# Kernel tuning notes

Measured on AMD Instinct MI355X. Metric: run time of the kernel, lower is better.

## Reference

```python
import jax, jax.numpy as jnp
import numpy as np

L, H, E, CUTOFF = 3, 128, 20, 5.0
N_NODES, N_EDGES = 10000, 160000
NUM_EMBED = 119


def _linear(key, fin, fout):
    kw, kb = jax.random.split(key)
    s = 1.0 / np.sqrt(fin)
    W = jax.random.uniform(kw, (fin, fout), minval=-s, maxval=s, dtype=jnp.float32)
    b = jax.random.uniform(kb, (fout,), minval=-s, maxval=s, dtype=jnp.float32)
    return W, b


def _stack(key, fin, fout):
    Ws, bs = zip(*[_linear(k, fin, fout) for k in jax.random.split(key, L)])
    return jnp.stack(Ws), jnp.stack(bs)


def setup_inputs() -> dict:
    key = jax.random.key(0)
    ks = jax.random.split(key, 14)
    z = jax.random.randint(ks[0], (N_NODES,), 0, NUM_EMBED)
    edge = jax.random.randint(ks[1], (N_EDGES, 2), 0, N_NODES)
    edge_diff = jax.random.normal(ks[2], (N_EDGES, 3), dtype=jnp.float32) * 1.5
    edge_dist = jnp.linalg.norm(edge_diff, axis=-1) + 1e-2  # consistent unit vectors, strictly > 0
    embed = jax.random.normal(ks[3], (NUM_EMBED, H), dtype=jnp.float32)
    msg_filter_w, msg_filter_b = _stack(ks[4], E, 3 * H)
    msg_w1, msg_b1 = _stack(ks[5], H, H)
    msg_w2, msg_b2 = _stack(ks[6], H, 3 * H)
    upd_U_w, upd_U_b = _stack(ks[7], H, H)
    upd_V_w, upd_V_b = _stack(ks[8], H, H)
    upd_w1, upd_b1 = _stack(ks[9], 2 * H, H)
    upd_w2, upd_b2 = _stack(ks[10], H, 3 * H)
    ro_w1, ro_b1 = _linear(ks[11], H, H)
    ro_w2, ro_b2 = _linear(ks[12], H, H)
    return dict(z=z, edge=edge, edge_diff=edge_diff, edge_dist=edge_dist, embed=embed,
                msg_filter_w=msg_filter_w, msg_filter_b=msg_filter_b,
                msg_w1=msg_w1, msg_b1=msg_b1, msg_w2=msg_w2, msg_b2=msg_b2,
                upd_U_w=upd_U_w, upd_U_b=upd_U_b, upd_V_w=upd_V_w, upd_V_b=upd_V_b,
                upd_w1=upd_w1, upd_b1=upd_b1, upd_w2=upd_w2, upd_b2=upd_b2,
                ro_w1=ro_w1, ro_b1=ro_b1, ro_w2=ro_w2, ro_b2=ro_b2)


def _silu(x):
    return x * jax.nn.sigmoid(x)


def reference(z, edge, edge_diff, edge_dist, embed,
              msg_filter_w, msg_filter_b, msg_w1, msg_b1, msg_w2, msg_b2,
              upd_U_w, upd_U_b, upd_V_w, upd_V_b, upd_w1, upd_b1, upd_w2, upd_b2,
              ro_w1, ro_b1, ro_w2, ro_b2):
    N = z.shape[0]
    pi = jnp.asarray(np.pi, dtype=edge_dist.dtype)
    # sinc radial basis: sin(n*pi*d/cutoff)/d, n=1..E  -> [E_edges, E]
    n = jnp.arange(1, E + 1, dtype=edge_dist.dtype)
    rbf = jnp.sin(edge_dist[:, None] * n * pi / CUTOFF) / edge_dist[:, None]
    # cosine cutoff [E_edges]
    fcut = jnp.where(edge_dist < CUTOFF, 0.5 * (jnp.cos(pi * edge_dist / CUTOFF) + 1.0), 0.0)
    unit = edge_diff / edge_dist[:, None]  # [E_edges, 3]
    src = edge[:, 1]
    dst = edge[:, 0]

    node_scalar = embed[z]                                       # [N, H]
    node_vector = jnp.zeros((N, 3, H), dtype=edge_diff.dtype)    # [N, 3, H]

    for l in range(L):
        # --- message ---
        filter_w = (rbf @ msg_filter_w[l] + msg_filter_b[l]) * fcut[:, None]   # [E_edges, 3H]
        scalar_out = _silu(node_scalar @ msg_w1[l] + msg_b1[l]) @ msg_w2[l] + msg_b2[l]  # [N, 3H]
        filter_out = filter_w * scalar_out[src]                                 # gather + mul
        gate_sv, gate_ev, msg_s = jnp.split(filter_out, 3, axis=1)
        msg_v = node_vector[src] * gate_sv[:, None, :] + gate_ev[:, None, :] * unit[:, :, None]
        node_scalar = node_scalar + jax.ops.segment_sum(msg_s, dst, num_segments=N)
        node_vector = node_vector + jax.ops.segment_sum(msg_v, dst, num_segments=N)
        # --- update ---
        Uv = node_vector @ upd_U_w[l] + upd_U_b[l]   # [N, 3, H]
        Vv = node_vector @ upd_V_w[l] + upd_V_b[l]
        Vv_norm = jnp.linalg.norm(Vv, axis=1)        # [N, H]
        mlp_in = jnp.concatenate((Vv_norm, node_scalar), axis=1)
        mlp_out = _silu(mlp_in @ upd_w1[l] + upd_b1[l]) @ upd_w2[l] + upd_b2[l]
        a_vv, a_sv, a_ss = jnp.split(mlp_out, 3, axis=1)
        node_vector = node_vector + a_vv[:, None, :] * Uv
        node_scalar = node_scalar + a_sv * jnp.sum(Uv * Vv, axis=1) + a_ss

    # readout MLP
    return _silu(node_scalar @ ro_w1 + ro_b1) @ ro_w2 + ro_b2
```

## Files before the change

kernel.cpp:

```cpp
#include <hip/hip_runtime.h>
#include <hip/hip_bf16.h>

typedef __hip_bfloat16 bf16;
typedef __attribute__((ext_vector_type(8))) short bf16x8;
typedef __attribute__((ext_vector_type(4))) float f32x4;

#define H 128
#define F3H 384
#define E_RBF 20
#define NLAYER 3

__device__ __forceinline__ float silu_f(float x) { return x / (1.0f + __expf(-x)); }
__device__ __forceinline__ float b2f(bf16 x) { return __bfloat162float(x); }

constexpr float PI_F = 3.14159265358979323846f;
constexpr float CUT = 5.0f;

__global__ __launch_bounds__(256) void csr_hist(
    const int* __restrict__ edge, int* __restrict__ cnt, int nE) {
  int e = blockIdx.x * blockDim.x + threadIdx.x;
  if (e < nE) atomicAdd(&cnt[edge[2 * e]], 1);
}

__global__ __launch_bounds__(1024) void csr_scan(
    const int* __restrict__ cnt, int* __restrict__ rowstart, int* __restrict__ cur, int N) {
  __shared__ int part[1024];
  int t = threadIdx.x;
  int chunk = (N + 1023) / 1024;
  int lo = t * chunk; if (lo > N) lo = N;
  int hi = lo + chunk; if (hi > N) hi = N;
  int s = 0;
  for (int i = lo; i < hi; i++) s += cnt[i];
  part[t] = s;
  __syncthreads();
  for (int off = 1; off < 1024; off <<= 1) {
    int v = (t >= off) ? part[t - off] : 0;
    __syncthreads();
    part[t] += v;
    __syncthreads();
  }
  int r = (t == 0) ? 0 : part[t - 1];
  for (int i = lo; i < hi; i++) { rowstart[i] = r; cur[i] = r; r += cnt[i]; }
}

__global__ __launch_bounds__(256) void csr_fill_pack(
    const int* __restrict__ edge, int* __restrict__ cur,
    const float* __restrict__ edist, const float* __restrict__ ediff,
    int* __restrict__ srcs, float* __restrict__ geo, int nE) {
  int e = blockIdx.x * blockDim.x + threadIdx.x;
  if (e >= nE) return;
  int d = edge[2 * e];
  int p = atomicAdd(&cur[d], 1);
  srcs[p] = edge[2 * e + 1];
  float dd = edist[e];
  float inv = 1.0f / dd;
  float th = dd * (PI_F / CUT);
  float s1 = sinf(th), c1 = cosf(th);
  float fc = (dd < CUT) ? 0.5f * (c1 + 1.0f) : 0.0f;
  float* g = geo + (size_t)p * 24;
  float twoc = 2.0f * c1;
  float skp = 0.0f, sk = s1;
  #pragma unroll
  for (int k = 0; k < E_RBF; k++) {
    g[k] = sk * inv * fc;
    float nx = twoc * sk - skp;
    skp = sk; sk = nx;
  }
  g[20] = ediff[3 * (size_t)e] * inv;
  g[21] = ediff[3 * (size_t)e + 1] * inv;
  g[22] = ediff[3 * (size_t)e + 2] * inv;
  g[23] = fc;
}

__device__ __forceinline__ void pack_w_item(
    const float* __restrict__ Wu, const float* __restrict__ Wv,
    bf16* __restrict__ wp, int t) {
  int lane = t & 63;
  int c    = (t >> 6) & 7;
  int kb   = (t >> 9) & 3;
  int mat  = (t >> 11) & 1;
  int l    = t >> 12;
  const float* src = (mat ? Wv : Wu) + (size_t)l * H * H;
  bf16* dst = wp + ((size_t)(l * 2 + mat) * 16384) + (((kb * 8 + c) * 64 + lane) * 8);
  int quad = lane >> 4;
  int n = c * 16 + (lane & 15);
  #pragma unroll
  for (int j = 0; j < 8; j++) {
    int k = kb * 32 + quad * 8 + j;
    dst[j] = __float2bfloat16(src[(size_t)k * H + n]);
  }
}

__device__ __forceinline__ void pack_b_item(
    const float* __restrict__ src, bf16* __restrict__ dst,
    int K, int ncols, int t) {
  int kblocks = K >> 5, ncols16 = ncols >> 4;
  int lane = t & 63;
  int idx = t >> 6;
  int c = idx % ncols16; idx /= ncols16;
  int kb = idx % kblocks; idx /= kblocks;
  int l = idx;
  const float* s = src + (size_t)l * K * ncols;
  bf16* d = dst + (size_t)l * K * ncols + (((kb * ncols16 + c) * 64 + lane) * 8);
  int quad = lane >> 4;
  int n = c * 16 + (lane & 15);
  #pragma unroll
  for (int j = 0; j < 8; j++) {
    int k = kb * 32 + quad * 8 + j;
    d[j] = __float2bfloat16(s[(size_t)k * ncols + n]);
  }
}

__global__ __launch_bounds__(256) void pack_all(
    const float* __restrict__ Wu, const float* __restrict__ Wv, bf16* __restrict__ wpack,
    const float* __restrict__ uw1, bf16* __restrict__ wp_m1,
    const float* __restrict__ uw2, bf16* __restrict__ wp_m2,
    const float* __restrict__ mw1, bf16* __restrict__ wp_sm1,
    const float* __restrict__ mw2, bf16* __restrict__ wp_sm2,
    const float* __restrict__ rw1, bf16* __restrict__ wp_ro1,
    const float* __restrict__ rw2, bf16* __restrict__ wp_ro2,
    const int* __restrict__ z, const float* __restrict__ embed,
    float* __restrict__ ns, bf16* __restrict__ ns16,
    int* __restrict__ cnt, int N) {
  const int T0 = 12288;
  const int T1 = T0 + 12288;
  const int T2 = T1 + 18432;
  const int T3 = T2 + 6144;
  const int T4 = T3 + 18432;
  const int T5 = T4 + 2048;
  const int T6 = T5 + 2048;
  const int TN = T6 + N * H;
  const int TT = TN + N;
  for (int t = blockIdx.x * blockDim.x + threadIdx.x; t < TT; t += gridDim.x * blockDim.x) {
    if (t < T0)      pack_w_item(Wu, Wv, wpack, t);
    else if (t < T1) pack_b_item(uw1, wp_m1, 256, 128, t - T0);
    else if (t < T2) pack_b_item(uw2, wp_m2, 128, 384, t - T1);
    else if (t < T3) pack_b_item(mw1, wp_sm1, 128, 128, t - T2);
    else if (t < T4) pack_b_item(mw2, wp_sm2, 128, 384, t - T3);
    else if (t < T5) pack_b_item(rw1, wp_ro1, 128, 128, t - T4);
    else if (t < T6) pack_b_item(rw2, wp_ro2, 128, 128, t - T5);
    else if (t < TN) {
      int u = t - T6;
      int i = u >> 7, h = u & 127;
      float v = embed[(size_t)z[i] * H + h];
      ns[(size_t)i * H + h] = v;
      ns16[(size_t)i * H + h] = __float2bfloat16(v);
    } else {
      cnt[t - TN] = 0;
    }
  }
}

__global__ __launch_bounds__(256) void mlp_msg(
    const bf16* __restrict__ A, const bf16* __restrict__ Wp1,
    const float* __restrict__ b1, const bf16* __restrict__ Wp2,
    const float* __restrict__ b2, bf16* __restrict__ so, int M) {
  __shared__ bf16 m1l[32][136];
  int wave = threadIdx.x >> 6, lane = threadIdx.x & 63;
  int rowg = wave >> 1, ch = wave & 1;
  int r0 = blockIdx.x * 32 + rowg * 16;
  int quad = lane >> 4, nn = lane & 15;
  int arow = r0 + nn; if (arow >= M) arow = M - 1;
  f32x4 acc[4] = {};
  for (int kb = 0; kb < 4; kb++) {
    bf16x8 af = *(const bf16x8*)&A[(size_t)arow * H + kb * 32 + quad * 8];
    #pragma unroll
    for (int c = 0; c < 4; c++) {
      int cg = ch * 4 + c;
      bf16x8 bw = *(const bf16x8*)&Wp1[(((kb * 8 + cg) * 64) + lane) * 8];
      acc[c] = __builtin_amdgcn_mfma_f32_16x16x32_bf16(af, bw, acc[c], 0, 0, 0);
    }
  }
  #pragma unroll
  for (int c = 0; c < 4; c++) {
    int n = (ch * 4 + c) * 16 + nn;
    float bb = b1[n];
    #pragma unroll
    for (int r = 0; r < 4; r++) {
      int lr = rowg * 16 + quad * 4 + r;
      m1l[lr][n] = __float2bfloat16(silu_f(acc[c][r] + bb));
    }
  }
  __syncthreads();
  f32x4 a0[4] = {}, a1[4] = {}, a2[4] = {};
  for (int kb = 0; kb < 4; kb++) {
    bf16x8 af = *(const bf16x8*)&m1l[rowg * 16 + nn][kb * 32 + quad * 8];
    #pragma unroll
    for (int c = 0; c < 4; c++) {
      int cg = ch * 4 + c;
      bf16x8 b0 = *(const bf16x8*)&Wp2[(((kb * 24 + cg) * 64) + lane) * 8];
      bf16x8 b1v = *(const bf16x8*)&Wp2[(((kb * 24 + cg + 8) * 64) + lane) * 8];
      bf16x8 b2v = *(const bf16x8*)&Wp2[(((kb * 24 + cg + 16) * 64) + lane) * 8];
      a0[c] = __builtin_amdgcn_mfma_f32_16x16x32_bf16(af, b0, a0[c], 0, 0, 0);
      a1[c] = __builtin_amdgcn_mfma_f32_16x16x32_bf16(af, b1v, a1[c], 0, 0, 0);
      a2[c] = __builtin_amdgcn_mfma_f32_16x16x32_bf16(af, b2v, a2[c], 0, 0, 0);
    }
  }
  #pragma unroll
  for (int c = 0; c < 4; c++) {
    int n = (ch * 4 + c) * 16 + nn;
    float bb0 = b2[n], bb1 = b2[H + n], bb2 = b2[2 * H + n];
    #pragma unroll
    for (int r = 0; r < 4; r++) {
      int row = r0 + quad * 4 + r;
      if (row < M) {
        so[(size_t)row * F3H + n]           = __float2bfloat16(a0[c][r] + bb0);
        so[(size_t)row * F3H + H + n]       = __float2bfloat16(a1[c][r] + bb1);
        so[(size_t)row * F3H + 2 * H + n]   = __float2bfloat16(a2[c][r] + bb2);
      }
    }
  }
}

__global__ __launch_bounds__(384) void uv_upd(
    const bf16* __restrict__ A, const bf16* __restrict__ Wpuv,
    const float* __restrict__ bu, const float* __restrict__ bv,
    const bf16* __restrict__ nsmsg,
    const bf16* __restrict__ Wp1, const float* __restrict__ b1,
    const bf16* __restrict__ Wp2, const float* __restrict__ b2,
    float* __restrict__ ns, bf16* __restrict__ ns16,
    float* __restrict__ nv, bf16* __restrict__ nvb16, int N) {
  __shared__ float Uv_l[96][132];
  __shared__ float Vv_l[96][132];
  __shared__ bf16 vn_l[32][136];
  __shared__ bf16 m1l[32][136];
  int wave = threadIdx.x >> 6;
  int lane = threadIdx.x & 63;
  int quad = lane >> 4, nn = lane & 15;
  int M3 = 3 * N;

  {
    int r0 = blockIdx.x * 96 + wave * 16;
    int arow = r0 + nn; if (arow >= M3) arow = M3 - 1;
    f32x4 accu[8] = {};
    f32x4 accv[8] = {};
    for (int kb = 0; kb < 4; kb++) {
      bf16x8 af = *(const bf16x8*)&A[(size_t)arow * H + kb * 32 + quad * 8];
      #pragma unroll
      for (int c = 0; c < 8; c++) {
        bf16x8 bfu = *(const bf16x8*)&Wpuv[(((kb * 8 + c) * 64) + lane) * 8];
        bf16x8 bfv = *(const bf16x8*)&Wpuv[16384 + (((kb * 8 + c) * 64) + lane) * 8];
        accu[c] = __builtin_amdgcn_mfma_f32_16x16x32_bf16(af, bfu, accu[c], 0, 0, 0);
        accv[c] = __builtin_amdgcn_mfma_f32_16x16x32_bf16(af, bfv, accv[c], 0, 0, 0);
      }
    }
    #pragma unroll
    for (int c = 0; c < 8; c++) {
      int n = c * 16 + nn;
      float bub = bu[n], bvb = bv[n];
      #pragma unroll
      for (int r = 0; r < 4; r++) {
        int lr = wave * 16 + quad * 4 + r;
        Uv_l[lr][n] = accu[c][r] + bub;
        Vv_l[lr][n] = accv[c][r] + bvb;
      }
    }
  }
  __syncthreads();

  for (int t = threadIdx.x; t < 32 * H; t += 384) {
    int node = t >> 7, hh = t & 127;
    float v0 = Vv_l[node * 3][hh];
    float v1 = Vv_l[node * 3 + 1][hh];
    float v2 = Vv_l[node * 3 + 2][hh];
    vn_l[node][hh] = __float2bfloat16(sqrtf(v0 * v0 + v1 * v1 + v2 * v2));
  }
  __syncthreads();

  int rowg = wave >> 1, ch = wave & 1;
  int r0n = blockIdx.x * 32 + rowg * 16;
  int arown = r0n + nn; if (arown >= N) arown = N - 1;
  if (wave < 4) {
    f32x4 acc[4] = {};
    for (int kb = 0; kb < 8; kb++) {
      bf16x8 af;
      if (kb < 4) af = *(const bf16x8*)&vn_l[rowg * 16 + nn][kb * 32 + quad * 8];
      else        af = *(const bf16x8*)&nsmsg[(size_t)arown * H + (kb - 4) * 32 + quad * 8];
      #pragma unroll
      for (int c = 0; c < 4; c++) {
        int cg = ch * 4 + c;
        bf16x8 bw = *(const bf16x8*)&Wp1[(((kb * 8 + cg) * 64) + lane) * 8];
        acc[c] = __builtin_amdgcn_mfma_f32_16x16x32_bf16(af, bw, acc[c], 0, 0, 0);
      }
    }
    #pragma unroll
    for (int c = 0; c < 4; c++) {
      int n = (ch * 4 + c) * 16 + nn;
      float bb = b1[n];
      #pragma unroll
      for (int r = 0; r < 4; r++) {
        int lr = rowg * 16 + quad * 4 + r;
        m1l[lr][n] = __float2bfloat16(silu_f(acc[c][r] + bb));
      }
    }
  }
  __syncthreads();

  if (wave < 4) {
    f32x4 aav[4] = {}, aas[4] = {}, asz[4] = {};
    for (int kb = 0; kb < 4; kb++) {
      bf16x8 af = *(const bf16x8*)&m1l[rowg * 16 + nn][kb * 32 + quad * 8];
      #pragma unroll
      for (int c = 0; c < 4; c++) {
        int cg = ch * 4 + c;
        bf16x8 b0 = *(const bf16x8*)&Wp2[(((kb * 24 + cg) * 64) + lane) * 8];
        bf16x8 b1v = *(const bf16x8*)&Wp2[(((kb * 24 + cg + 8) * 64) + lane) * 8];
        bf16x8 b2v = *(const bf16x8*)&Wp2[(((kb * 24 + cg + 16) * 64) + lane) * 8];
        aav[c] = __builtin_amdgcn_mfma_f32_16x16x32_bf16(af, b0, aav[c], 0, 0, 0);
        aas[c] = __builtin_amdgcn_mfma_f32_16x16x32_bf16(af, b1v, aas[c], 0, 0, 0);
        asz[c] = __builtin_amdgcn_mfma_f32_16x16x32_bf16(af, b2v, asz[c], 0, 0, 0);
      }
    }
    #pragma unroll
    for (int c = 0; c < 4; c++) {
      int n = (ch * 4 + c) * 16 + nn;
      float bav = b2[n], bas = b2[H + n], bss = b2[2 * H + n];
      #pragma unroll
      for (int r = 0; r < 4; r++) {
        int row = r0n + quad * 4 + r;
        if (row < N) {
          int lrn = rowg * 16 + quad * 4 + r;
          float avv = aav[c][r] + bav;
          float asv = aas[c][r] + bas;
          float ass = asz[c][r] + bss;
          float u0 = Uv_l[lrn * 3 + 0][n];
          float u1 = Uv_l[lrn * 3 + 1][n];
          float u2 = Uv_l[lrn * 3 + 2][n];
          float v0 = Vv_l[lrn * 3 + 0][n];
          float v1 = Vv_l[lrn * 3 + 1][n];
          float v2 = Vv_l[lrn * 3 + 2][n];
          float dot = u0 * v0 + u1 * v1 + u2 * v2;
          float ns_new = ns[(size_t)row * H + n] + asv * dot + ass;
          ns[(size_t)row * H + n] = ns_new;
          ns16[(size_t)row * H + n] = __float2bfloat16(ns_new);
          float n0 = nv[(size_t)(3 * row + 0) * H + n] + avv * u0;
          float n1 = nv[(size_t)(3 * row + 1) * H + n] + avv * u1;
          float n2 = nv[(size_t)(3 * row + 2) * H + n] + avv * u2;
          nv[(size_t)(3 * row + 0) * H + n] = n0;
          nv[(size_t)(3 * row + 1) * H + n] = n1;
          nv[(size_t)(3 * row + 2) * H + n] = n2;
          nvb16[(size_t)(3 * row + 0) * H + n] = __float2bfloat16(n0);
          nvb16[(size_t)(3 * row + 1) * H + n] = __float2bfloat16(n1);
          nvb16[(size_t)(3 * row + 2) * H + n] = __float2bfloat16(n2);
        }
      }
    }
  }
}

__global__ __launch_bounds__(256) void mlp_ro(
    const bf16* __restrict__ A, const bf16* __restrict__ Wp1,
    const float* __restrict__ b1, const bf16* __restrict__ Wp2,
    const float* __restrict__ b2, float* __restrict__ out, int M) {
  __shared__ bf16 m1l[32][136];
  int wave = threadIdx.x >> 6, lane = threadIdx.x & 63;
  int rowg = wave >> 1, ch = wave & 1;
  int r0 = blockIdx.x * 32 + rowg * 16;
  int quad = lane >> 4, nn = lane & 15;
  int arow = r0 + nn; if (arow >= M) arow = M - 1;
  f32x4 acc[4] = {};
  for (int kb = 0; kb < 4; kb++) {
    bf16x8 af = *(const bf16x8*)&A[(size_t)arow * H + kb * 32 + quad * 8];
    #pragma unroll
    for (int c = 0; c < 4; c++) {
      int cg = ch * 4 + c;
      bf16x8 bw = *(const bf16x8*)&Wp1[(((kb * 8 + cg) * 64) + lane) * 8];
      acc[c] = __builtin_amdgcn_mfma_f32_16x16x32_bf16(af, bw, acc[c], 0, 0, 0);
    }
  }
  #pragma unroll
  for (int c = 0; c < 4; c++) {
    int n = (ch * 4 + c) * 16 + nn;
    float bb = b1[n];
    #pragma unroll
    for (int r = 0; r < 4; r++) {
      int lr = rowg * 16 + quad * 4 + r;
      m1l[lr][n] = __float2bfloat16(silu_f(acc[c][r] + bb));
    }
  }
  __syncthreads();
  f32x4 a2[4] = {};
  for (int kb = 0; kb < 4; kb++) {
    bf16x8 af = *(const bf16x8*)&m1l[rowg * 16 + nn][kb * 32 + quad * 8];
    #pragma unroll
    for (int c = 0; c < 4; c++) {
      int cg = ch * 4 + c;
      bf16x8 bw = *(const bf16x8*)&Wp2[(((kb * 8 + cg) * 64) + lane) * 8];
      a2[c] = __builtin_amdgcn_mfma_f32_16x16x32_bf16(af, bw, a2[c], 0, 0, 0);
    }
  }
  #pragma unroll
  for (int c = 0; c < 4; c++) {
    int n = (ch * 4 + c) * 16 + nn;
    float bb = b2[n];
    #pragma unroll
    for (int r = 0; r < 4; r++) {
      int row = r0 + quad * 4 + r;
      if (row < M) out[(size_t)row * H + n] = a2[c][r] + bb;
    }
  }
}

template<bool HASNV>
__global__ __launch_bounds__(128, 4) void message3(
    const int* __restrict__ srcs, const int* __restrict__ rowstart,
    const int* __restrict__ cnt, const float* __restrict__ geo,
    const float* __restrict__ Wf, const float* __restrict__ bfb,
    const bf16* __restrict__ so, const bf16* __restrict__ nvb16,
    const float* __restrict__ nvA,
    float* __restrict__ ns, float* __restrict__ nvB,
    bf16* __restrict__ nvmsg16, bf16* __restrict__ nsmsg, int N) {
  int i = blockIdx.x;
  int h = threadIdx.x;

  float wf0[E_RBF], wf1[E_RBF], wf2[E_RBF];
  #pragma unroll
  for (int k = 0; k < E_RBF; k++) {
    wf0[k] = Wf[k * F3H + h];
    wf1[k] = Wf[k * F3H + H + h];
    wf2[k] = Wf[k * F3H + 2 * H + h];
  }
  float bb0 = bfb[h], bb1 = bfb[H + h], bb2 = bfb[2 * H + h];

  float accs = 0.0f, a0 = 0.0f, a1 = 0.0f, a2 = 0.0f;
  int jlo = rowstart[i], jhi = jlo + cnt[i];
  int j = jlo;
  for (; j + 1 < jhi; j += 2) {
    int s0 = srcs[j];
    int s1 = srcs[j + 1];
    const bf16* sop0 = so + (size_t)s0 * F3H;
    const bf16* sop1 = so + (size_t)s1 * F3H;
    float sA0 = b2f(sop0[h]), sB0 = b2f(sop0[H + h]), sC0 = b2f(sop0[2 * H + h]);
    float sA1 = b2f(sop1[h]), sB1 = b2f(sop1[H + h]), sC1 = b2f(sop1[2 * H + h]);
    float nA0, nB0, nC0, nA1, nB1, nC1;
    if (HASNV) {
      const bf16* nvp0 = nvb16 + (size_t)s0 * F3H;
      const bf16* nvp1 = nvb16 + (size_t)s1 * F3H;
      nA0 = b2f(nvp0[h]); nB0 = b2f(nvp0[H + h]); nC0 = b2f(nvp0[2 * H + h]);
      nA1 = b2f(nvp1[h]); nB1 = b2f(nvp1[H + h]); nC1 = b2f(nvp1[2 * H + h]);
    }

    {
      const float* g = geo + (size_t)j * 24;
      float gg[24];
      #pragma unroll
      for (int q = 0; q < 6; q++) *(float4*)&gg[4 * q] = *(const float4*)&g[4 * q];
      float fc = gg[23];
      float f0 = bb0 * fc, f1 = bb1 * fc, f2 = bb2 * fc;
      #pragma unroll
      for (int k = 0; k < E_RBF; k++) {
        float rk = gg[k];
        f0 += rk * wf0[k];
        f1 += rk * wf1[k];
        f2 += rk * wf2[k];
      }
      float u0 = gg[20], u1 = gg[21], u2 = gg[22];
      float gsv = f0 * sA0;
      float gev = f1 * sB0;
      accs += f2 * sC0;
      if (HASNV) {
        a0 += nA0 * gsv + gev * u0;
        a1 += nB0 * gsv + gev * u1;
        a2 += nC0 * gsv + gev * u2;
      } else {
        a0 += gev * u0;
        a1 += gev * u1;
        a2 += gev * u2;
      }
    }
    {
      const float* g = geo + (size_t)(j + 1) * 24;
      float gg[24];
      #pragma unroll
      for (int q = 0; q < 6; q++) *(float4*)&gg[4 * q] = *(const float4*)&g[4 * q];
      float fc = gg[23];
      float f0 = bb0 * fc, f1 = bb1 * fc, f2 = bb2 * fc;
      #pragma unroll
      for (int k = 0; k < E_RBF; k++) {
        float rk = gg[k];
        f0 += rk * wf0[k];
        f1 += rk * wf1[k];
        f2 += rk * wf2[k];
      }
      float u0 = gg[20], u1 = gg[21], u2 = gg[22];
      float gsv = f0 * sA1;
      float gev = f1 * sB1;
      accs += f2 * sC1;
      if (HASNV) {
        a0 += nA1 * gsv + gev * u0;
        a1 += nB1 * gsv + gev * u1;
        a2 += nC1 * gsv + gev * u2;
      } else {
        a0 += gev * u0;
        a1 += gev * u1;
        a2 += gev * u2;
      }
    }
  }
  if (j < jhi) {
    int src = srcs[j];
    const float* g = geo + (size_t)j * 24;
    float gg[24];
    #pragma unroll
    for (int q = 0; q < 6; q++) *(float4*)&gg[4 * q] = *(const float4*)&g[4 * q];
    float fc = gg[23];
    float f0 = bb0 * fc, f1 = bb1 * fc, f2 = bb2 * fc;
    #pragma unroll
    for (int k = 0; k < E_RBF; k++) {
      float rk = gg[k];
      f0 += rk * wf0[k];
      f1 += rk * wf1[k];
      f2 += rk * wf2[k];
    }
    float u0 = gg[20], u1 = gg[21], u2 = gg[22];
    const bf16* sop = so + (size_t)src * F3H;
    float gsv = f0 * b2f(sop[h]);
    float gev = f1 * b2f(sop[H + h]);
    accs += f2 * b2f(sop[2 * H + h]);
    if (HASNV) {
      const bf16* nvp = nvb16 + (size_t)src * F3H;
      a0 += b2f(nvp[h])         * gsv + gev * u0;
      a1 += b2f(nvp[H + h])     * gsv + gev * u1;
      a2 += b2f(nvp[2 * H + h]) * gsv + gev * u2;
    } else {
      a0 += gev * u0;
      a1 += gev * u1;
      a2 += gev * u2;
    }
  }

  float ns_new = ns[(size_t)i * H + h] + accs;
  ns[(size_t)i * H + h] = ns_new;
  nsmsg[(size_t)i * H + h] = __float2bfloat16(ns_new);
  float o0, o1, o2;
  if (HASNV) {
    const float* nvi = nvA + (size_t)i * F3H;
    o0 = nvi[h] + a0;
    o1 = nvi[H + h] + a1;
    o2 = nvi[2 * H + h] + a2;
  } else {
    o0 = a0; o1 = a1; o2 = a2;
  }
  nvB[(size_t)i * F3H + h]         = o0;
  nvB[(size_t)i * F3H + H + h]     = o1;
  nvB[(size_t)i * F3H + 2 * H + h] = o2;
  nvmsg16[(size_t)i * F3H + h]         = __float2bfloat16(o0);
  nvmsg16[(size_t)i * F3H + H + h]     = __float2bfloat16(o1);
  nvmsg16[(size_t)i * F3H + 2 * H + h] = __float2bfloat16(o2);
}

extern "C" void kernel_launch(void* const* d_in, const int* in_sizes, int n_in,
                              void* d_out, int out_size, void* d_ws, size_t ws_size,
                              hipStream_t stream) {
  const int*   z     = (const int*)d_in[0];
  const int*   edge  = (const int*)d_in[1];
  const float* ediff = (const float*)d_in[2];
  const float* edist = (const float*)d_in[3];
  const float* embed = (const float*)d_in[4];
  const float* mfw   = (const float*)d_in[5];
  const float* mfb   = (const float*)d_in[6];
  const float* mw1   = (const float*)d_in[7];
  const float* mb1   = (const float*)d_in[8];
  const float* mw2   = (const float*)d_in[9];
  const float* mb2   = (const float*)d_in[10];
  const float* uUw   = (const float*)d_in[11];
  const float* uUb   = (const float*)d_in[12];
  const float* uVw   = (const float*)d_in[13];
  const float* uVb   = (const float*)d_in[14];
  const float* uw1   = (const float*)d_in[15];
  const float* ub1   = (const float*)d_in[16];
  const float* uw2   = (const float*)d_in[17];
  const float* ub2   = (const float*)d_in[18];
  const float* rw1   = (const float*)d_in[19];
  const float* rb1   = (const float*)d_in[20];
  const float* rw2   = (const float*)d_in[21];
  const float* rb2   = (const float*)d_in[22];

  const int N  = in_sizes[0];
  const int nE = in_sizes[3];

  float* ws = (float*)d_ws;
  size_t off = 0;
  float* ns      = ws + off; off += (size_t)N * H;
  float* nvA     = ws + off; off += (size_t)N * F3H;
  float* nvB     = ws + off; off += (size_t)N * F3H;
  float* geo     = ws + off; off += (size_t)nE * 24;
  bf16* so       = (bf16*)(ws + off); off += (size_t)N * F3H / 2;
  bf16* nvb16    = (bf16*)(ws + off); off += (size_t)N * F3H / 2;
  bf16* nvmsg16  = (bf16*)(ws + off); off += (size_t)N * F3H / 2;
  bf16* nsmsg    = (bf16*)(ws + off); off += (size_t)N * 64;
  bf16* ns16     = (bf16*)(ws + off); off += (size_t)N * 64;
  bf16* wpack    = (bf16*)(ws + off); off += 3 * 2 * 16384 / 2;
  bf16* wp_m1    = (bf16*)(ws + off); off += 3 * 256 * 128 / 2;
  bf16* wp_m2    = (bf16*)(ws + off); off += 3 * 128 * 384 / 2;
  bf16* wp_sm1   = (bf16*)(ws + off); off += 3 * 128 * 128 / 2;
  bf16* wp_sm2   = (bf16*)(ws + off); off += 3 * 128 * 384 / 2;
  bf16* wp_ro1   = (bf16*)(ws + off); off += 128 * 128 / 2;
  bf16* wp_ro2   = (bf16*)(ws + off); off += 128 * 128 / 2;
  int* srcs     = (int*)(ws + off); off += nE;
  int* cnt      = (int*)(ws + off); off += N;
  int* rowstart = (int*)(ws + off); off += N;
  int* cur      = (int*)(ws + off); off += N;

  const int tilesN = (N + 31) / 32;

  pack_all<<<1024, 256, 0, stream>>>(
      uUw, uVw, wpack, uw1, wp_m1, uw2, wp_m2, mw1, wp_sm1, mw2, wp_sm2,
      rw1, wp_ro1, rw2, wp_ro2, z, embed, ns, ns16, cnt, N);
  csr_hist<<<(nE + 255) / 256, 256, 0, stream>>>(edge, cnt, nE);
  csr_scan<<<1, 1024, 0, stream>>>(cnt, rowstart, cur, N);
  csr_fill_pack<<<(nE + 255) / 256, 256, 0, stream>>>(edge, cur, edist, ediff, srcs, geo, nE);

  float* nv_cur = nvA;
  float* nv_nxt = nvB;
  for (int l = 0; l < NLAYER; l++) {
    mlp_msg<<<tilesN, 256, 0, stream>>>(
        ns16, wp_sm1 + (size_t)l * 128 * 128, mb1 + (size_t)l * H,
        wp_sm2 + (size_t)l * 128 * 384, mb2 + (size_t)l * F3H, so, N);

    if (l == 0)
      message3<false><<<N, H, 0, stream>>>(srcs, rowstart, cnt, geo,
                                           mfw + (size_t)l * E_RBF * F3H, mfb + (size_t)l * F3H,
                                           so, nvb16, nv_cur, ns, nv_nxt, nvmsg16, nsmsg, N);
    else
      message3<true><<<N, H, 0, stream>>>(srcs, rowstart, cnt, geo,
                                          mfw + (size_t)l * E_RBF * F3H, mfb + (size_t)l * F3H,
                                          so, nvb16, nv_cur, ns, nv_nxt, nvmsg16, nsmsg, N);

    uv_upd<<<tilesN, 384, 0, stream>>>(
        nvmsg16, wpack + (size_t)l * 2 * 16384,
        uUb + (size_t)l * H, uVb + (size_t)l * H,
        nsmsg,
        wp_m1 + (size_t)l * 256 * 128, ub1 + (size_t)l * H,
        wp_m2 + (size_t)l * 128 * 384, ub2 + (size_t)l * F3H,
        ns, ns16, nv_nxt, nvb16, N);

    float* t = nv_cur; nv_cur = nv_nxt; nv_nxt = t;
  }

  mlp_ro<<<tilesN, 256, 0, stream>>>(
      ns16, wp_ro1, rb1, wp_ro2, rb2, (float*)d_out, N);
}
```

Measured before the change: 483.2 us.

## Halve uv_upd tile to 16 nodes and split U/V GEMM across waves

The fused update kernel now handles 16 nodes per block instead of 32, doubling the grid and halving shared memory per block. The six waves are redistributed: three compute U and three compute V for the 48 vector rows, and all six waves share the eight column groups of the two MLP stages instead of only four waves working. Fewer accumulators per wave plus launch bounds of 3 blocks per CU aim to raise occupancy and parallelism. In exchange, each block reloads the weight fragments for half as many rows, and the MLP stages are unbalanced (two waves do two groups).

```diff
diff --git a/kernel.cpp b/kernel.cpp
--- a/kernel.cpp
+++ b/kernel.cpp
@@ -212,7 +212,7 @@
   }
 }
 
-__global__ __launch_bounds__(384) void uv_upd(
+__global__ __launch_bounds__(384, 3) void uv_upd(
     const bf16* __restrict__ A, const bf16* __restrict__ Wpuv,
     const float* __restrict__ bu, const float* __restrict__ bv,
     const bf16* __restrict__ nsmsg,
@@ -220,45 +220,46 @@
     const bf16* __restrict__ Wp2, const float* __restrict__ b2,
     float* __restrict__ ns, bf16* __restrict__ ns16,
     float* __restrict__ nv, bf16* __restrict__ nvb16, int N) {
-  __shared__ float Uv_l[96][132];
-  __shared__ float Vv_l[96][132];
-  __shared__ bf16 vn_l[32][136];
-  __shared__ bf16 m1l[32][136];
+  __shared__ float Uv_l[48][132];
+  __shared__ float Vv_l[48][132];
+  __shared__ bf16 vn_l[16][136];
+  __shared__ bf16 m1l[16][136];
   int wave = threadIdx.x >> 6;
   int lane = threadIdx.x & 63;
   int quad = lane >> 4, nn = lane & 15;
   int M3 = 3 * N;
 
   {
-    int r0 = blockIdx.x * 96 + wave * 16;
+    int wt = (wave >= 3) ? wave - 3 : wave;
+    bool isV = wave >= 3;
+    int r0 = blockIdx.x * 48 + wt * 16;
     int arow = r0 + nn; if (arow >= M3) arow = M3 - 1;
-    f32x4 accu[8] = {};
-    f32x4 accv[8] = {};
+    const bf16* Wb = Wpuv + (isV ? 16384 : 0);
+    f32x4 acc[8] = {};
     for (int kb = 0; kb < 4; kb++) {
       bf16x8 af = *(const bf16x8*)&A[(size_t)arow * H + kb * 32 + quad * 8];
       #pragma unroll
       for (int c = 0; c < 8; c++) {
-        bf16x8 bfu = *(const bf16x8*)&Wpuv[(((kb * 8 + c) * 64) + lane) * 8];
-        bf16x8 bfv = *(const bf16x8*)&Wpuv[16384 + (((kb * 8 + c) * 64) + lane) * 8];
-        accu[c] = __builtin_amdgcn_mfma_f32_16x16x32_bf16(af, bfu, accu[c], 0, 0, 0);
-        accv[c] = __builtin_amdgcn_mfma_f32_16x16x32_bf16(af, bfv, accv[c], 0, 0, 0);
-      }
-    }
+        bf16x8 bw = *(const bf16x8*)&Wb[(((kb * 8 + c) * 64) + lane) * 8];
+        acc[c] = __builtin_amdgcn_mfma_f32_16x16x32_bf16(af, bw, acc[c], 0, 0, 0);
+      }
+    }
+    const float* bias = isV ? bv : bu;
     #pragma unroll
     for (int c = 0; c < 8; c++) {
       int n = c * 16 + nn;
-      float bub = bu[n], bvb = bv[n];
+      float bb = bias[n];
       #pragma unroll
       for (int r = 0; r < 4; r++) {
-        int lr = wave * 16 + quad * 4 + r;
-        Uv_l[lr][n] = accu[c][r] + bub;
-        Vv_l[lr][n] = accv[c][r] + bvb;
+        int lr = wt * 16 + quad * 4 + r;
+        if (isV) Vv_l[lr][n] = acc[c][r] + bb;
+        else     Uv_l[lr][n] = acc[c][r] + bb;
       }
     }
   }
   __syncthreads();
 
-  for (int t = threadIdx.x; t < 32 * H; t += 384) {
+  for (int t = threadIdx.x; t < 16 * H; t += 384) {
     int node = t >> 7, hh = t & 127;
     float v0 = Vv_l[node * 3][hh];
     float v1 = Vv_l[node * 3 + 1][hh];
@@ -267,82 +268,66 @@
   }
   __syncthreads();
 
-  int rowg = wave >> 1, ch = wave & 1;
-  int r0n = blockIdx.x * 32 + rowg * 16;
+  int r0n = blockIdx.x * 16;
   int arown = r0n + nn; if (arown >= N) arown = N - 1;
-  if (wave < 4) {
-    f32x4 acc[4] = {};
+  for (int g = wave; g < 8; g += 6) {
+    f32x4 acc = {};
     for (int kb = 0; kb < 8; kb++) {
       bf16x8 af;
-      if (kb < 4) af = *(const bf16x8*)&vn_l[rowg * 16 + nn][kb * 32 + quad * 8];
+      if (kb < 4) af = *(const bf16x8*)&vn_l[nn][kb * 32 + quad * 8];
       else        af = *(const bf16x8*)&nsmsg[(size_t)arown * H + (kb - 4) * 32 + quad * 8];
-      #pragma unroll
-      for (int c = 0; c < 4; c++) {
-        int cg = ch * 4 + c;
-        bf16x8 bw = *(const bf16x8*)&Wp1[(((kb * 8 + cg) * 64) + lane) * 8];
-        acc[c] = __builtin_amdgcn_mfma_f32_16x16x32_bf16(af, bw, acc[c], 0, 0, 0);
-      }
-    }
-    #pragma unroll
-    for (int c = 0; c < 4; c++) {
-      int n = (ch * 4 + c) * 16 + nn;
-      float bb = b1[n];
-      #pragma unroll
-      for (int r = 0; r < 4; r++) {
-        int lr = rowg * 16 + quad * 4 + r;
-        m1l[lr][n] = __float2bfloat16(silu_f(acc[c][r] + bb));
-      }
+      bf16x8 bw = *(const bf16x8*)&Wp1[(((kb * 8 + g) * 64) + lane) * 8];
+      acc = __builtin_amdgcn_mfma_f32_16x16x32_bf16(af, bw, acc, 0, 0, 0);
+    }
+    int n = g * 16 + nn;
+    float bb = b1[n];
+    #pragma unroll
+    for (int r = 0; r < 4; r++) {
+      m1l[quad * 4 + r][n] = __float2bfloat16(silu_f(acc[r] + bb));
     }
   }
   __syncthreads();
 
-  if (wave < 4) {
-    f32x4 aav[4] = {}, aas[4] = {}, asz[4] = {};
+  for (int g = wave; g < 8; g += 6) {
+    f32x4 aav = {}, aas = {}, asz = {};
     for (int kb = 0; kb < 4; kb++) {
-      bf16x8 af = *(const bf16x8*)&m1l[rowg * 16 + nn][kb * 32 + quad * 8];
-      #pragma unroll
-      for (int c = 0; c < 4; c++) {
-        int cg = ch * 4 + c;
-        bf16x8 b0 = *(const bf16x8*)&Wp2[(((kb * 24 + cg) * 64) + lane) * 8];
-        bf16x8 b1v = *(const bf16x8*)&Wp2[(((kb * 24 + cg + 8) * 64) + lane) * 8];
-        bf16x8 b2v = *(const bf16x8*)&Wp2[(((kb * 24 + cg + 16) * 64) + lane) * 8];
-        aav[c] = __builtin_amdgcn_mfma_f32_16x16x32_bf16(af, b0, aav[c], 0, 0, 0);
-        aas[c] = __builtin_amdgcn_mfma_f32_16x16x32_bf16(af, b1v, aas[c], 0, 0, 0);
-        asz[c] = __builtin_amdgcn_mfma_f32_16x16x32_bf16(af, b2v, asz[c], 0, 0, 0);
-      }
-    }
-    #pragma unroll
-    for (int c = 0; c < 4; c++) {
-      int n = (ch * 4 + c) * 16 + nn;
-      float bav = b2[n], bas = b2[H + n], bss = b2[2 * H + n];
-      #pragma unroll
-      for (int r = 0; r < 4; r++) {
-        int row = r0n + quad * 4 + r;
-        if (row < N) {
-          int lrn = rowg * 16 + quad * 4 + r;
-          float avv = aav[c][r] + bav;
-          float asv = aas[c][r] + bas;
-          float ass = asz[c][r] + bss;
-          float u0 = Uv_l[lrn * 3 + 0][n];
-          float u1 = Uv_l[lrn * 3 + 1][n];
-          float u2 = Uv_l[lrn * 3 + 2][n];
-          float v0 = Vv_l[lrn * 3 + 0][n];
-          float v1 = Vv_l[lrn * 3 + 1][n];
-          float v2 = Vv_l[lrn * 3 + 2][n];
-          float dot = u0 * v0 + u1 * v1 + u2 * v2;
-          float ns_new = ns[(size_t)row * H + n] + asv * dot + ass;
-          ns[(size_t)row * H + n] = ns_new;
-          ns16[(size_t)row * H + n] = __float2bfloat16(ns_new);
-          float n0 = nv[(size_t)(3 * row + 0) * H + n] + avv * u0;
-          float n1 = nv[(size_t)(3 * row + 1) * H + n] + avv * u1;
-          float n2 = nv[(size_t)(3 * row + 2) * H + n] + avv * u2;
-          nv[(size_t)(3 * row + 0) * H + n] = n0;
-          nv[(size_t)(3 * row + 1) * H + n] = n1;
-          nv[(size_t)(3 * row + 2) * H + n] = n2;
-          nvb16[(size_t)(3 * row + 0) * H + n] = __float2bfloat16(n0);
-          nvb16[(size_t)(3 * row + 1) * H + n] = __float2bfloat16(n1);
-          nvb16[(size_t)(3 * row + 2) * H + n] = __float2bfloat16(n2);
-        }
+      bf16x8 af = *(const bf16x8*)&m1l[nn][kb * 32 + quad * 8];
+      bf16x8 b0 = *(const bf16x8*)&Wp2[(((kb * 24 + g) * 64) + lane) * 8];
+      bf16x8 b1v = *(const bf16x8*)&Wp2[(((kb * 24 + g + 8) * 64) + lane) * 8];
+      bf16x8 b2v = *(const bf16x8*)&Wp2[(((kb * 24 + g + 16) * 64) + lane) * 8];
+      aav = __builtin_amdgcn_mfma_f32_16x16x32_bf16(af, b0, aav, 0, 0, 0);
+      aas = __builtin_amdgcn_mfma_f32_16x16x32_bf16(af, b1v, aas, 0, 0, 0);
+      asz = __builtin_amdgcn_mfma_f32_16x16x32_bf16(af, b2v, asz, 0, 0, 0);
+    }
+    int n = g * 16 + nn;
+    float bav = b2[n], bas = b2[H + n], bss = b2[2 * H + n];
+    #pragma unroll
+    for (int r = 0; r < 4; r++) {
+      int row = r0n + quad * 4 + r;
+      if (row < N) {
+        int lrn = quad * 4 + r;
+        float avv = aav[r] + bav;
+        float asv = aas[r] + bas;
+        float ass = asz[r] + bss;
+        float u0 = Uv_l[lrn * 3 + 0][n];
+        float u1 = Uv_l[lrn * 3 + 1][n];
+        float u2 = Uv_l[lrn * 3 + 2][n];
+        float v0 = Vv_l[lrn * 3 + 0][n];
+        float v1 = Vv_l[lrn * 3 + 1][n];
+        float v2 = Vv_l[lrn * 3 + 2][n];
+        float dot = u0 * v0 + u1 * v1 + u2 * v2;
+        float ns_new = ns[(size_t)row * H + n] + asv * dot + ass;
+        ns[(size_t)row * H + n] = ns_new;
+        ns16[(size_t)row * H + n] = __float2bfloat16(ns_new);
+        float n0 = nv[(size_t)(3 * row + 0) * H + n] + avv * u0;
+        float n1 = nv[(size_t)(3 * row + 1) * H + n] + avv * u1;
+        float n2 = nv[(size_t)(3 * row + 2) * H + n] + avv * u2;
+        nv[(size_t)(3 * row + 0) * H + n] = n0;
+        nv[(size_t)(3 * row + 1) * H + n] = n1;
+        nv[(size_t)(3 * row + 2) * H + n] = n2;
+        nvb16[(size_t)(3 * row + 0) * H + n] = __float2bfloat16(n0);
+        nvb16[(size_t)(3 * row + 1) * H + n] = __float2bfloat16(n1);
+        nvb16[(size_t)(3 * row + 2) * H + n] = __float2bfloat16(n2);
       }
     }
   }
@@ -603,6 +588,7 @@
   int* cur      = (int*)(ws + off); off += N;
 
   const int tilesN = (N + 31) / 32;
+  const int tilesUV = (N + 15) / 16;
 
   pack_all<<<1024, 256, 0, stream>>>(
       uUw, uVw, wpack, uw1, wp_m1, uw2, wp_m2, mw1, wp_sm1, mw2, wp_sm2,
@@ -627,7 +613,7 @@
                                           mfw + (size_t)l * E_RBF * F3H, mfb + (size_t)l * F3H,
                                           so, nvb16, nv_cur, ns, nv_nxt, nvmsg16, nsmsg, N);
 
-    uv_upd<<<tilesN, 384, 0, stream>>>(
+    uv_upd<<<tilesUV, 384, 0, stream>>>(
         nvmsg16, wpack + (size_t)l * 2 * 16384,
         uUb + (size_t)l * H, uVb + (size_t)l * H,
         nsmsg,
```

New measurement: 453.8 us. 6.1% less time.
